# Kernel optimization log

Measured on AMD Instinct MI355X. Metric: run time of the kernel, lower is better.

The kernel has to match this reference:

```python
import jax, jax.numpy as jnp
import numpy as np

N_NODES = 100000


def _gcn_layer(x, W, b, src, dst, norm, n):
    # x: [N, Din] -> [N, Dout]; PyG GCNConv: transform then normalized scatter-add
    h = x @ W                                   # [N, Dout]
    msgs = h[src] * norm[:, None]               # [E+N, Dout] gather + scale
    agg = jax.ops.segment_sum(msgs, dst, num_segments=n)  # scatter-add to dst
    return agg + b


def setup_inputs() -> dict:
    key = jax.random.key(0)
    k1, k2, k3, k4 = jax.random.split(key, 4)
    n, e = N_NODES, 800000
    din, dh, dout = 128, 128, 64
    x = jax.random.normal(k1, (n, din), dtype=jnp.float32)
    edge_index = jax.random.randint(k2, (2, e), 0, n, dtype=jnp.int64)
    W1 = jax.random.normal(k3, (din, dh), dtype=jnp.float32) * (1.0 / np.sqrt(din))
    b1 = jnp.zeros((dh,), dtype=jnp.float32)
    W2 = jax.random.normal(k4, (dh, dout), dtype=jnp.float32) * (1.0 / np.sqrt(dh))
    b2 = jnp.zeros((dout,), dtype=jnp.float32)
    return {"x": x, "edge_index": edge_index, "W1": W1, "b1": b1, "W2": W2, "b2": b2}


def reference(x, edge_index, W1, b1, W2, b2):
    n = x.shape[0]
    loops = jnp.arange(n, dtype=edge_index.dtype)
    src = jnp.concatenate([edge_index[0], loops])  # [E+N]
    dst = jnp.concatenate([edge_index[1], loops])  # [E+N]
    # symmetric normalization D^-1/2 (A+I) D^-1/2 (degree counted at dst, as in PyG)
    deg = jax.ops.segment_sum(jnp.ones_like(src, dtype=x.dtype), dst, num_segments=n)
    dinv = jnp.where(deg > 0, jax.lax.rsqrt(jnp.maximum(deg, 1e-12)), 0.0)
    norm = dinv[src] * dinv[dst]                   # [E+N]

    h = _gcn_layer(x, W1, b1, src, dst, norm, n)
    h = jax.nn.elu(h)
    # dropout(p=0.5) is identity in eval mode
    out = _gcn_layer(h, W2, b2, src, dst, norm, n)
    return out
```

## Files before the change

### kernel.cpp

```cpp
#include <hip/hip_runtime.h>


typedef __attribute__((ext_vector_type(8))) short bf16x8;
typedef __attribute__((ext_vector_type(4))) float f32x4;

static __device__ __forceinline__ unsigned short f2bf(float f) {
    unsigned u = __builtin_bit_cast(unsigned, f);
    u += 0x7fffu + ((u >> 16) & 1u);
    return (unsigned short)(u >> 16);
}
static __device__ __forceinline__ float bflo(unsigned u) {
    return __builtin_bit_cast(float, u << 16);
}
static __device__ __forceinline__ f32x4 bfquad(uint2 v) {
    f32x4 r;
    r[0] = bflo(v.x); r[1] = __builtin_bit_cast(float, v.x);
    r[2] = bflo(v.y); r[3] = __builtin_bit_cast(float, v.y);
    return r;
}

#define CHUNK 4096
#define NBUCKP 512

__global__ __launch_bounds__(256) void k_hist(const int* __restrict__ dst,
        int* __restrict__ ghist, int E, int nblk,
        const float* __restrict__ W1, const float* __restrict__ W2,
        unsigned short* __restrict__ W1t, unsigned short* __restrict__ W2t) {
    __shared__ int h[NBUCKP];
    const int tid = threadIdx.x, b = blockIdx.x;
    if (b >= nblk) {
        int i = (b - nblk) * 256 + tid;
        if (i < 128 * 128) {
            int n = i >> 7, k = i & 127;
            W1t[i] = f2bf(W1[k * 128 + n]);
        }
        int j = i - 128 * 128;
        if (j >= 0 && j < 64 * 128) {
            int n = j >> 7, k = j & 127;
            W2t[j] = f2bf(W2[k * 64 + n]);
        }
        return;
    }
    h[tid] = 0; h[tid + 256] = 0;
    __syncthreads();
    const int base = b * CHUNK;
#pragma unroll
    for (int i = 0; i < CHUNK / 256; ++i) {
        int e = base + i * 256 + tid;
        if (e < E) atomicAdd(&h[dst[e] >> 8], 1);
    }
    __syncthreads();
    ghist[tid * nblk + b] = h[tid];
    ghist[(tid + 256) * nblk + b] = h[tid + 256];
}

__global__ __launch_bounds__(256) void k_part(const int* __restrict__ v,
                                              int* __restrict__ part, int L) {
    __shared__ int s[256];
    int tid = threadIdx.x;
    int i = blockIdx.x * 256 + tid;
    s[tid] = (i < L) ? v[i] : 0;
    __syncthreads();
    for (int o = 128; o > 0; o >>= 1) {
        if (tid < o) s[tid] += s[tid + o];
        __syncthreads();
    }
    if (tid == 0) part[blockIdx.x] = s[0];
}

__global__ __launch_bounds__(512) void k_scanpart(int* __restrict__ part, int nb) {
    __shared__ int s[512];
    int tid = threadIdx.x;
    int v = (tid < nb) ? part[tid] : 0;
    s[tid] = v;
    __syncthreads();
    for (int off = 1; off < 512; off <<= 1) {
        int t = (tid >= off) ? s[tid - off] : 0;
        __syncthreads();
        s[tid] += t;
        __syncthreads();
    }
    if (tid < nb) part[tid] = s[tid] - v;
}

__global__ __launch_bounds__(256) void k_scan_apply(int* __restrict__ v,
        const int* __restrict__ part, int L) {
    __shared__ int s[256];
    int tid = threadIdx.x;
    int i = blockIdx.x * 256 + tid;
    int x = (i < L) ? v[i] : 0;
    s[tid] = x;
    __syncthreads();
    for (int off = 1; off < 256; off <<= 1) {
        int t = (tid >= off) ? s[tid - off] : 0;
        __syncthreads();
        s[tid] += t;
        __syncthreads();
    }
    if (i < L) v[i] = part[blockIdx.x] + s[tid] - x;
}

__global__ __launch_bounds__(256) void k_scatter_part(const int* __restrict__ src,
        const int* __restrict__ dst, const int* __restrict__ S,
        unsigned* __restrict__ eb, int E, int nblk) {
    __shared__ int cur[NBUCKP];
    const int tid = threadIdx.x, b = blockIdx.x;
    cur[tid] = S[tid * nblk + b];
    cur[tid + 256] = S[(tid + 256) * nblk + b];
    __syncthreads();
    const int base = b * CHUNK;
#pragma unroll
    for (int i = 0; i < CHUNK / 256; ++i) {
        int e = base + i * 256 + tid;
        if (e < E) {
            int s = src[e], d = dst[e];
            int pos = atomicAdd(&cur[d >> 8], 1);
            eb[pos] = ((unsigned)(d & 255) << 24) | (unsigned)s;
        }
    }
}

__global__ __launch_bounds__(256) void k_bucket_csr(const unsigned* __restrict__ eb,
        const int* __restrict__ S, int* __restrict__ row_ptr,
        float* __restrict__ dinv, int* __restrict__ col, int E, int nblk, int N) {
    __shared__ int h[256], sc[256], cur[256];
    const int tid = threadIdx.x, k = blockIdx.x;
    const int bstart = S[k * nblk];
    const int bend   = S[(k + 1) * nblk];
    h[tid] = 0;
    __syncthreads();
    for (int e = bstart + tid; e < bend; e += 256)
        atomicAdd(&h[eb[e] >> 24], 1);
    __syncthreads();
    int v = h[tid];
    sc[tid] = v;
    __syncthreads();
    for (int off = 1; off < 256; off <<= 1) {
        int t = (tid >= off) ? sc[tid - off] : 0;
        __syncthreads();
        sc[tid] += t;
        __syncthreads();
    }
    int excl = sc[tid] - v;
    int n = k * 256 + tid;
    if (n < N) {
        row_ptr[n] = bstart + excl;
        dinv[n] = rsqrtf((float)v + 1.0f);
        if (n == N - 1) row_ptr[N] = bstart + excl + v;
    }
    cur[tid] = excl;
    __syncthreads();
    for (int e = bstart + tid; e < bend; e += 256) {
        unsigned ed = eb[e];
        int pos = bstart + atomicAdd(&cur[ed >> 24], 1);
        col[pos] = (int)(ed & 0xFFFFFFu);
    }
}

template<int NC, bool ABF16>
__global__ __launch_bounds__(256) void k_gemm(const void* __restrict__ Av,
        const unsigned short* __restrict__ Wt, const float* __restrict__ dinv,
        unsigned short* __restrict__ C, int M) {
    __shared__ unsigned short sA[64][136];
    __shared__ unsigned short sW[NC][136];
    const int tid  = threadIdx.x;
    const int lane = tid & 63;
    const int wave = tid >> 6;
    const int row0 = blockIdx.x * 64;

    if (ABF16) {
        const uint4* A = (const uint4*)Av;
#pragma unroll
        for (int p = 0; p < 4; ++p) {
            int c = tid + p * 256;
            int row = c >> 4, cc = c & 15;
            uint4 v = make_uint4(0u, 0u, 0u, 0u);
            if (row0 + row < M) v = A[(size_t)(row0 + row) * 16 + cc];
            *(uint4*)&sA[row][cc * 8] = v;
        }
    } else {
        const float* A = (const float*)Av;
#pragma unroll
        for (int p = 0; p < 8; ++p) {
            int c = tid + p * 256;
            int row = c >> 5, c4 = (c & 31) * 4;
            float4 v = make_float4(0.f, 0.f, 0.f, 0.f);
            if (row0 + row < M) v = *(const float4*)&A[(size_t)(row0 + row) * 128 + c4];
            ushort4 o;
            o.x = f2bf(v.x); o.y = f2bf(v.y); o.z = f2bf(v.z); o.w = f2bf(v.w);
            *(ushort4*)&sA[row][c4] = o;
        }
    }
    {
        const uint4* W4 = (const uint4*)Wt;
#pragma unroll
        for (int p = 0; p < NC / 16; ++p) {
            int c = tid + p * 256;
            int n = c >> 4, cc = c & 15;
            *(uint4*)&sW[n][cc * 8] = W4[c];
        }
    }
    __syncthreads();

    constexpr int CT = NC / 64;
    const int colbase = wave * (NC / 4);
    const int frow = lane & 15;
    const int fk   = (lane >> 4) * 8;

    f32x4 acc[4][CT];
#pragma unroll
    for (int rt = 0; rt < 4; ++rt)
#pragma unroll
        for (int ct = 0; ct < CT; ++ct) acc[rt][ct] = (f32x4){0.f, 0.f, 0.f, 0.f};

#pragma unroll
    for (int kk = 0; kk < 128; kk += 32) {
        bf16x8 a[4], b[CT];
#pragma unroll
        for (int rt = 0; rt < 4; ++rt)
            a[rt] = *(const bf16x8*)&sA[rt * 16 + frow][kk + fk];
#pragma unroll
        for (int ct = 0; ct < CT; ++ct)
            b[ct] = *(const bf16x8*)&sW[colbase + ct * 16 + frow][kk + fk];
#pragma unroll
        for (int rt = 0; rt < 4; ++rt)
#pragma unroll
            for (int ct = 0; ct < CT; ++ct)
                acc[rt][ct] = __builtin_amdgcn_mfma_f32_16x16x32_bf16(
                    a[rt], b[ct], acc[rt][ct], 0, 0, 0);
    }

    const int crow = (lane >> 4) * 4;
#pragma unroll
    for (int rt = 0; rt < 4; ++rt) {
        int grow = row0 + rt * 16 + crow;
#pragma unroll
        for (int r = 0; r < 4; ++r) {
            if (grow + r < M) {
                float s = dinv[grow + r];
#pragma unroll
                for (int ct = 0; ct < CT; ++ct) {
                    int gcol = colbase + ct * 16 + (lane & 15);
                    C[(size_t)(grow + r) * NC + gcol] = f2bf(acc[rt][ct][r] * s);
                }
            }
        }
    }
}

template<bool ELU>
__global__ __launch_bounds__(256) void k_gather128(const unsigned* __restrict__ H,
        const int* __restrict__ row_ptr, const int* __restrict__ col,
        const float* __restrict__ dinv, const float* __restrict__ bias,
        unsigned* __restrict__ outbf, int N) {
    const int wave = threadIdx.x >> 6, lane = threadIdx.x & 63;
    const int n = blockIdx.x * 4 + wave;
    if (n >= N) return;
    const int beg = row_ptr[n], end = row_ptr[n + 1];
    const int half = lane >> 5;
    const int s = lane & 31;
    f32x4 acc = (f32x4){0.f, 0.f, 0.f, 0.f};

    if (half == 0) {
        uint2 v = *(const uint2*)&H[(size_t)n * 64 + 2 * s];
        acc += bfquad(v);
    }
    int j = beg + half;
    for (; j + 6 < end; j += 8) {
        int c0 = col[j], c1 = col[j + 2], c2 = col[j + 4], c3 = col[j + 6];
        uint2 v0 = *(const uint2*)&H[(size_t)c0 * 64 + 2 * s];
        uint2 v1 = *(const uint2*)&H[(size_t)c1 * 64 + 2 * s];
        uint2 v2 = *(const uint2*)&H[(size_t)c2 * 64 + 2 * s];
        uint2 v3 = *(const uint2*)&H[(size_t)c3 * 64 + 2 * s];
        acc += bfquad(v0);
        acc += bfquad(v1);
        acc += bfquad(v2);
        acc += bfquad(v3);
    }
    if (j < end) {
        const int e1 = end - 1;
        int j1 = j + 2, j2 = j + 4;
        int c0 = col[j];
        int c1 = col[j1 <= e1 ? j1 : e1];
        int c2 = col[j2 <= e1 ? j2 : e1];
        float w1 = (j1 < end) ? 1.f : 0.f;
        float w2 = (j2 < end) ? 1.f : 0.f;
        uint2 v0 = *(const uint2*)&H[(size_t)c0 * 64 + 2 * s];
        uint2 v1 = *(const uint2*)&H[(size_t)c1 * 64 + 2 * s];
        uint2 v2 = *(const uint2*)&H[(size_t)c2 * 64 + 2 * s];
        acc += bfquad(v0);
        acc += bfquad(v1) * w1;
        acc += bfquad(v2) * w2;
    }

    float a0 = acc[0], a1 = acc[1], a2 = acc[2], a3 = acc[3];
    a0 += __shfl_xor(a0, 32); a1 += __shfl_xor(a1, 32);
    a2 += __shfl_xor(a2, 32); a3 += __shfl_xor(a3, 32);
    if (half == 0) {
        float sc = dinv[n];
        float4 b = *(const float4*)&bias[4 * s];
        float o0 = fmaf(a0, sc, b.x), o1 = fmaf(a1, sc, b.y);
        float o2 = fmaf(a2, sc, b.z), o3 = fmaf(a3, sc, b.w);
        if (ELU) {
            o0 = o0 > 0.f ? o0 : expm1f(o0);
            o1 = o1 > 0.f ? o1 : expm1f(o1);
            o2 = o2 > 0.f ? o2 : expm1f(o2);
            o3 = o3 > 0.f ? o3 : expm1f(o3);
        }
        uint2 o;
        o.x = (unsigned)f2bf(o0) | ((unsigned)f2bf(o1) << 16);
        o.y = (unsigned)f2bf(o2) | ((unsigned)f2bf(o3) << 16);
        *(uint2*)&outbf[(size_t)n * 64 + 2 * s] = o;
    }
}

__global__ __launch_bounds__(256) void k_gather64(const unsigned* __restrict__ H,
        const int* __restrict__ row_ptr, const int* __restrict__ col,
        const float* __restrict__ dinv, const float* __restrict__ bias,
        float* __restrict__ out, int N) {
    const int wave = threadIdx.x >> 6, lane = threadIdx.x & 63;
    const int n = blockIdx.x * 4 + wave;
    if (n >= N) return;
    const int beg = row_ptr[n], end = row_ptr[n + 1];
    const int q = lane >> 4;
    const int s = lane & 15;
    f32x4 acc = (f32x4){0.f, 0.f, 0.f, 0.f};

    if (q == 0) {
        uint2 v = *(const uint2*)&H[(size_t)n * 32 + 2 * s];
        acc += bfquad(v);
    }
    int j = beg + q;
    for (; j + 12 < end; j += 16) {
        int c0 = col[j], c1 = col[j + 4], c2 = col[j + 8], c3 = col[j + 12];
        uint2 v0 = *(const uint2*)&H[(size_t)c0 * 32 + 2 * s];
        uint2 v1 = *(const uint2*)&H[(size_t)c1 * 32 + 2 * s];
        uint2 v2 = *(const uint2*)&H[(size_t)c2 * 32 + 2 * s];
        uint2 v3 = *(const uint2*)&H[(size_t)c3 * 32 + 2 * s];
        acc += bfquad(v0);
        acc += bfquad(v1);
        acc += bfquad(v2);
        acc += bfquad(v3);
    }
    if (j < end) {
        const int e1 = end - 1;
        int j1 = j + 4, j2 = j + 8;
        int c0 = col[j];
        int c1 = col[j1 <= e1 ? j1 : e1];
        int c2 = col[j2 <= e1 ? j2 : e1];
        float w1 = (j1 < end) ? 1.f : 0.f;
        float w2 = (j2 < end) ? 1.f : 0.f;
        uint2 v0 = *(const uint2*)&H[(size_t)c0 * 32 + 2 * s];
        uint2 v1 = *(const uint2*)&H[(size_t)c1 * 32 + 2 * s];
        uint2 v2 = *(const uint2*)&H[(size_t)c2 * 32 + 2 * s];
        acc += bfquad(v0);
        acc += bfquad(v1) * w1;
        acc += bfquad(v2) * w2;
    }

    float a0 = acc[0], a1 = acc[1], a2 = acc[2], a3 = acc[3];
    a0 += __shfl_xor(a0, 16); a1 += __shfl_xor(a1, 16);
    a2 += __shfl_xor(a2, 16); a3 += __shfl_xor(a3, 16);
    a0 += __shfl_xor(a0, 32); a1 += __shfl_xor(a1, 32);
    a2 += __shfl_xor(a2, 32); a3 += __shfl_xor(a3, 32);
    if (q == 0) {
        float sc = dinv[n];
        float4 b = *(const float4*)&bias[4 * s];
        float4 o;
        o.x = fmaf(a0, sc, b.x); o.y = fmaf(a1, sc, b.y);
        o.z = fmaf(a2, sc, b.z); o.w = fmaf(a3, sc, b.w);
        *(float4*)&out[(size_t)n * 64 + 4 * s] = o;
    }
}

extern "C" void kernel_launch(void* const* d_in, const int* in_sizes, int n_in,
                              void* d_out, int out_size, void* d_ws, size_t ws_size,
                              hipStream_t stream) {
    const float* x  = (const float*)d_in[0];
    const int*   ei = (const int*)d_in[1];
    const float* W1 = (const float*)d_in[2];
    const float* b1 = (const float*)d_in[3];
    const float* W2 = (const float*)d_in[4];
    const float* b2 = (const float*)d_in[5];
    float* out = (float*)d_out;

    const int N = in_sizes[0] / 128;
    const int E = in_sizes[1] / 2;
    const int* src = ei;
    const int* dst = ei + E;
    const int NPAD = (N + 63) & ~63;

    const int NBLK_A = (E + CHUNK - 1) / CHUNK;
    const int L      = NBUCKP * NBLK_A;
    const int NBLK_S = (L + 255) / 256;
    const int NBUCK  = (N + 255) / 256;

    unsigned off = 0;
    int* row_ptr    = (int*)d_ws + off;            off += NPAD + 64;
    float* dinv     = (float*)((int*)d_ws + off);  off += NPAD + 64;
    int* ghist      = (int*)d_ws + off;            off += (unsigned)((L + 63) & ~63);
    int* part       = (int*)d_ws + off;            off += 512;
    unsigned* eb    = (unsigned*)((int*)d_ws + off); off += (unsigned)((E + 63) & ~63);
    int* col        = (int*)d_ws + off;            off += (unsigned)((E + 63) & ~63);
    unsigned short* W1t = (unsigned short*)((int*)d_ws + off); off += 8192;
    unsigned short* W2t = (unsigned short*)((int*)d_ws + off); off += 4096;
    unsigned* H     = (unsigned*)((int*)d_ws + off); off += (unsigned)N * 64 + 64;
    unsigned* act   = (unsigned*)((int*)d_ws + off);

    k_hist<<<NBLK_A + 96, 256, 0, stream>>>(dst, ghist, E, NBLK_A, W1, W2, W1t, W2t);
    k_part<<<NBLK_S, 256, 0, stream>>>(ghist, part, L);
    k_scanpart<<<1, 512, 0, stream>>>(part, NBLK_S);
    k_scan_apply<<<NBLK_S, 256, 0, stream>>>(ghist, part, L);
    k_scatter_part<<<NBLK_A, 256, 0, stream>>>(src, dst, ghist, eb, E, NBLK_A);
    k_bucket_csr<<<NBUCK, 256, 0, stream>>>(eb, ghist, row_ptr, dinv, col, E, NBLK_A, N);

    k_gemm<128, false><<<(N + 63) / 64, 256, 0, stream>>>(x, W1t, dinv,
                                                          (unsigned short*)H, N);
    k_gather128<true><<<(N + 3) / 4, 256, 0, stream>>>(H, row_ptr, col, dinv, b1, act, N);

    k_gemm<64, true><<<(N + 63) / 64, 256, 0, stream>>>(act, W2t, dinv,
                                                        (unsigned short*)H, N);
    k_gather64<<<(N + 3) / 4, 256, 0, stream>>>(H, row_ptr, col, dinv, b2, out, N);
}
```

Measured before the change: 153.6 us.

## Cooperatively load neighbor indices and gather 16-byte rows in aggregation kernels

Both gather kernels now have each lane load one column index per 64-edge chunk, then broadcast it with shuffles. Each row gather uses 16-byte loads over fewer lanes, so more edges are in flight per wave (4 or 8 edge groups instead of 2 or 4). The self-loop is folded into the index stream rather than handled separately. The aim is to cut redundant index loads and raise memory-level parallelism in this latency-bound SpMM. In exchange it adds shuffles, masked tail iterations that still issue loads, and a deeper cross-lane reduction.

```diff
diff --git a/kernel.cpp b/kernel.cpp
--- a/kernel.cpp
+++ b/kernel.cpp
@@ -12,11 +12,8 @@
 static __device__ __forceinline__ float bflo(unsigned u) {
     return __builtin_bit_cast(float, u << 16);
 }
-static __device__ __forceinline__ f32x4 bfquad(uint2 v) {
-    f32x4 r;
-    r[0] = bflo(v.x); r[1] = __builtin_bit_cast(float, v.x);
-    r[2] = bflo(v.y); r[3] = __builtin_bit_cast(float, v.y);
-    return r;
+static __device__ __forceinline__ float bfraw(unsigned u) {
+    return __builtin_bit_cast(float, u);
 }
 
 #define CHUNK 4096
@@ -256,61 +253,71 @@
     const int wave = threadIdx.x >> 6, lane = threadIdx.x & 63;
     const int n = blockIdx.x * 4 + wave;
     if (n >= N) return;
-    const int beg = row_ptr[n], end = row_ptr[n + 1];
-    const int half = lane >> 5;
-    const int s = lane & 31;
-    f32x4 acc = (f32x4){0.f, 0.f, 0.f, 0.f};
-
-    if (half == 0) {
-        uint2 v = *(const uint2*)&H[(size_t)n * 64 + 2 * s];
-        acc += bfquad(v);
-    }
-    int j = beg + half;
-    for (; j + 6 < end; j += 8) {
-        int c0 = col[j], c1 = col[j + 2], c2 = col[j + 4], c3 = col[j + 6];
-        uint2 v0 = *(const uint2*)&H[(size_t)c0 * 64 + 2 * s];
-        uint2 v1 = *(const uint2*)&H[(size_t)c1 * 64 + 2 * s];
-        uint2 v2 = *(const uint2*)&H[(size_t)c2 * 64 + 2 * s];
-        uint2 v3 = *(const uint2*)&H[(size_t)c3 * 64 + 2 * s];
-        acc += bfquad(v0);
-        acc += bfquad(v1);
-        acc += bfquad(v2);
-        acc += bfquad(v3);
-    }
-    if (j < end) {
-        const int e1 = end - 1;
-        int j1 = j + 2, j2 = j + 4;
-        int c0 = col[j];
-        int c1 = col[j1 <= e1 ? j1 : e1];
-        int c2 = col[j2 <= e1 ? j2 : e1];
-        float w1 = (j1 < end) ? 1.f : 0.f;
-        float w2 = (j2 < end) ? 1.f : 0.f;
-        uint2 v0 = *(const uint2*)&H[(size_t)c0 * 64 + 2 * s];
-        uint2 v1 = *(const uint2*)&H[(size_t)c1 * 64 + 2 * s];
-        uint2 v2 = *(const uint2*)&H[(size_t)c2 * 64 + 2 * s];
-        acc += bfquad(v0);
-        acc += bfquad(v1) * w1;
-        acc += bfquad(v2) * w2;
-    }
-
-    float a0 = acc[0], a1 = acc[1], a2 = acc[2], a3 = acc[3];
-    a0 += __shfl_xor(a0, 32); a1 += __shfl_xor(a1, 32);
-    a2 += __shfl_xor(a2, 32); a3 += __shfl_xor(a3, 32);
-    if (half == 0) {
+    const int beg = row_ptr[n];
+    const int cnt = row_ptr[n + 1] - beg + 1;
+    const int g   = lane >> 4;
+    const int c16 = lane & 15;
+    f32x4 accA = (f32x4){0.f, 0.f, 0.f, 0.f};
+    f32x4 accB = (f32x4){0.f, 0.f, 0.f, 0.f};
+
+    for (int chunk = 0; chunk < cnt; chunk += 64) {
+        int t = chunk + lane;
+        int cidx = n;
+        if (t > 0 && t < cnt) cidx = col[beg + t - 1];
+        int m = cnt - chunk; if (m > 64) m = 64;
+        for (int it = 0; it < m; it += 8) {
+            int t0 = it + g, t1 = it + 4 + g;
+            int ca = __shfl(cidx, t0);
+            int cb = __shfl(cidx, t1);
+            float wa = (t0 < m) ? 1.f : 0.f;
+            float wb = (t1 < m) ? 1.f : 0.f;
+            uint4 va = *(const uint4*)&H[(size_t)ca * 64 + (c16 << 2)];
+            uint4 vb = *(const uint4*)&H[(size_t)cb * 64 + (c16 << 2)];
+            f32x4 qa, qb;
+            qa[0] = bflo(va.x); qa[1] = bfraw(va.x);
+            qa[2] = bflo(va.y); qa[3] = bfraw(va.y);
+            qb[0] = bflo(va.z); qb[1] = bfraw(va.z);
+            qb[2] = bflo(va.w); qb[3] = bfraw(va.w);
+            accA += qa * wa; accB += qb * wa;
+            qa[0] = bflo(vb.x); qa[1] = bfraw(vb.x);
+            qa[2] = bflo(vb.y); qa[3] = bfraw(vb.y);
+            qb[0] = bflo(vb.z); qb[1] = bfraw(vb.z);
+            qb[2] = bflo(vb.w); qb[3] = bfraw(vb.w);
+            accA += qa * wb; accB += qb * wb;
+        }
+    }
+
+#pragma unroll
+    for (int k2 = 0; k2 < 4; ++k2) {
+        accA[k2] += __shfl_xor(accA[k2], 16);
+        accB[k2] += __shfl_xor(accB[k2], 16);
+        accA[k2] += __shfl_xor(accA[k2], 32);
+        accB[k2] += __shfl_xor(accB[k2], 32);
+    }
+    if (g == 0) {
         float sc = dinv[n];
-        float4 b = *(const float4*)&bias[4 * s];
-        float o0 = fmaf(a0, sc, b.x), o1 = fmaf(a1, sc, b.y);
-        float o2 = fmaf(a2, sc, b.z), o3 = fmaf(a3, sc, b.w);
+        float4 b0 = *(const float4*)&bias[c16 * 8];
+        float4 b1 = *(const float4*)&bias[c16 * 8 + 4];
+        float o0 = fmaf(accA[0], sc, b0.x), o1 = fmaf(accA[1], sc, b0.y);
+        float o2 = fmaf(accA[2], sc, b0.z), o3 = fmaf(accA[3], sc, b0.w);
+        float o4 = fmaf(accB[0], sc, b1.x), o5 = fmaf(accB[1], sc, b1.y);
+        float o6 = fmaf(accB[2], sc, b1.z), o7 = fmaf(accB[3], sc, b1.w);
         if (ELU) {
             o0 = o0 > 0.f ? o0 : expm1f(o0);
             o1 = o1 > 0.f ? o1 : expm1f(o1);
             o2 = o2 > 0.f ? o2 : expm1f(o2);
             o3 = o3 > 0.f ? o3 : expm1f(o3);
-        }
-        uint2 o;
+            o4 = o4 > 0.f ? o4 : expm1f(o4);
+            o5 = o5 > 0.f ? o5 : expm1f(o5);
+            o6 = o6 > 0.f ? o6 : expm1f(o6);
+            o7 = o7 > 0.f ? o7 : expm1f(o7);
+        }
+        uint4 o;
         o.x = (unsigned)f2bf(o0) | ((unsigned)f2bf(o1) << 16);
         o.y = (unsigned)f2bf(o2) | ((unsigned)f2bf(o3) << 16);
-        *(uint2*)&outbf[(size_t)n * 64 + 2 * s] = o;
+        o.z = (unsigned)f2bf(o4) | ((unsigned)f2bf(o5) << 16);
+        o.w = (unsigned)f2bf(o6) | ((unsigned)f2bf(o7) << 16);
+        *(uint4*)&outbf[(size_t)n * 64 + (c16 << 2)] = o;
     }
 }
 
@@ -321,55 +328,60 @@
     const int wave = threadIdx.x >> 6, lane = threadIdx.x & 63;
     const int n = blockIdx.x * 4 + wave;
     if (n >= N) return;
-    const int beg = row_ptr[n], end = row_ptr[n + 1];
-    const int q = lane >> 4;
-    const int s = lane & 15;
-    f32x4 acc = (f32x4){0.f, 0.f, 0.f, 0.f};
-
-    if (q == 0) {
-        uint2 v = *(const uint2*)&H[(size_t)n * 32 + 2 * s];
-        acc += bfquad(v);
-    }
-    int j = beg + q;
-    for (; j + 12 < end; j += 16) {
-        int c0 = col[j], c1 = col[j + 4], c2 = col[j + 8], c3 = col[j + 12];
-        uint2 v0 = *(const uint2*)&H[(size_t)c0 * 32 + 2 * s];
-        uint2 v1 = *(const uint2*)&H[(size_t)c1 * 32 + 2 * s];
-        uint2 v2 = *(const uint2*)&H[(size_t)c2 * 32 + 2 * s];
-        uint2 v3 = *(const uint2*)&H[(size_t)c3 * 32 + 2 * s];
-        acc += bfquad(v0);
-        acc += bfquad(v1);
-        acc += bfquad(v2);
-        acc += bfquad(v3);
-    }
-    if (j < end) {
-        const int e1 = end - 1;
-        int j1 = j + 4, j2 = j + 8;
-        int c0 = col[j];
-        int c1 = col[j1 <= e1 ? j1 : e1];
-        int c2 = col[j2 <= e1 ? j2 : e1];
-        float w1 = (j1 < end) ? 1.f : 0.f;
-        float w2 = (j2 < end) ? 1.f : 0.f;
-        uint2 v0 = *(const uint2*)&H[(size_t)c0 * 32 + 2 * s];
-        uint2 v1 = *(const uint2*)&H[(size_t)c1 * 32 + 2 * s];
-        uint2 v2 = *(const uint2*)&H[(size_t)c2 * 32 + 2 * s];
-        acc += bfquad(v0);
-        acc += bfquad(v1) * w1;
-        acc += bfquad(v2) * w2;
-    }
-
-    float a0 = acc[0], a1 = acc[1], a2 = acc[2], a3 = acc[3];
-    a0 += __shfl_xor(a0, 16); a1 += __shfl_xor(a1, 16);
-    a2 += __shfl_xor(a2, 16); a3 += __shfl_xor(a3, 16);
-    a0 += __shfl_xor(a0, 32); a1 += __shfl_xor(a1, 32);
-    a2 += __shfl_xor(a2, 32); a3 += __shfl_xor(a3, 32);
-    if (q == 0) {
+    const int beg = row_ptr[n];
+    const int cnt = row_ptr[n + 1] - beg + 1;
+    const int g  = lane >> 3;
+    const int c8 = lane & 7;
+    f32x4 accA = (f32x4){0.f, 0.f, 0.f, 0.f};
+    f32x4 accB = (f32x4){0.f, 0.f, 0.f, 0.f};
+
+    for (int chunk = 0; chunk < cnt; chunk += 64) {
+        int t = chunk + lane;
+        int cidx = n;
+        if (t > 0 && t < cnt) cidx = col[beg + t - 1];
+        int m = cnt - chunk; if (m > 64) m = 64;
+        for (int it = 0; it < m; it += 16) {
+            int t0 = it + g, t1 = it + 8 + g;
+            int ca = __shfl(cidx, t0);
+            int cb = __shfl(cidx, t1);
+            float wa = (t0 < m) ? 1.f : 0.f;
+            float wb = (t1 < m) ? 1.f : 0.f;
+            uint4 va = *(const uint4*)&H[(size_t)ca * 32 + (c8 << 2)];
+            uint4 vb = *(const uint4*)&H[(size_t)cb * 32 + (c8 << 2)];
+            f32x4 qa, qb;
+            qa[0] = bflo(va.x); qa[1] = bfraw(va.x);
+            qa[2] = bflo(va.y); qa[3] = bfraw(va.y);
+            qb[0] = bflo(va.z); qb[1] = bfraw(va.z);
+            qb[2] = bflo(va.w); qb[3] = bfraw(va.w);
+            accA += qa * wa; accB += qb * wa;
+            qa[0] = bflo(vb.x); qa[1] = bfraw(vb.x);
+            qa[2] = bflo(vb.y); qa[3] = bfraw(vb.y);
+            qb[0] = bflo(vb.z); qb[1] = bfraw(vb.z);
+            qb[2] = bflo(vb.w); qb[3] = bfraw(vb.w);
+            accA += qa * wb; accB += qb * wb;
+        }
+    }
+
+#pragma unroll
+    for (int k2 = 0; k2 < 4; ++k2) {
+        accA[k2] += __shfl_xor(accA[k2], 8);
+        accB[k2] += __shfl_xor(accB[k2], 8);
+        accA[k2] += __shfl_xor(accA[k2], 16);
+        accB[k2] += __shfl_xor(accB[k2], 16);
+        accA[k2] += __shfl_xor(accA[k2], 32);
+        accB[k2] += __shfl_xor(accB[k2], 32);
+    }
+    if (g == 0) {
         float sc = dinv[n];
-        float4 b = *(const float4*)&bias[4 * s];
-        float4 o;
-        o.x = fmaf(a0, sc, b.x); o.y = fmaf(a1, sc, b.y);
-        o.z = fmaf(a2, sc, b.z); o.w = fmaf(a3, sc, b.w);
-        *(float4*)&out[(size_t)n * 64 + 4 * s] = o;
+        float4 b0 = *(const float4*)&bias[c8 * 8];
+        float4 b1 = *(const float4*)&bias[c8 * 8 + 4];
+        float4 oa, ob;
+        oa.x = fmaf(accA[0], sc, b0.x); oa.y = fmaf(accA[1], sc, b0.y);
+        oa.z = fmaf(accA[2], sc, b0.z); oa.w = fmaf(accA[3], sc, b0.w);
+        ob.x = fmaf(accB[0], sc, b1.x); ob.y = fmaf(accB[1], sc, b1.y);
+        ob.z = fmaf(accB[2], sc, b1.z); ob.w = fmaf(accB[3], sc, b1.w);
+        *(float4*)&out[(size_t)n * 64 + c8 * 8]     = oa;
+        *(float4*)&out[(size_t)n * 64 + c8 * 8 + 4] = ob;
     }
 }
 
```

Result: slower. 159.4 us (+3.8%).
